# Kernel tuning notes

Measured on AMD Instinct MI355X. Metric: run time of the kernel, lower is better.

Reference implementation:

```python
import jax, jax.numpy as jnp
import numpy as np

N_NODES = 100000
N_EDGES = 1600000
IN_DIM, H1, H2, OUT_DIM = 128, 64, 32, 16


def setup_inputs() -> dict:
    key = jax.random.key(0)
    ks = jax.random.split(key, 9)
    x = jax.random.normal(ks[0], (N_NODES, IN_DIM), dtype=jnp.float32)
    edge_index = jax.random.randint(ks[1], (2, N_EDGES), 0, N_NODES, dtype=jnp.int64)
    # nn.Linear-style params (out_feats, in_feats) + bias
    def lin(k, o, i):
        bound = 1.0 / np.sqrt(i)
        kw, kb = jax.random.split(k)
        W = jax.random.uniform(kw, (o, i), jnp.float32, -bound, bound)
        b = jax.random.uniform(kb, (o,), jnp.float32, -bound, bound)
        return W, b
    W1, b1 = lin(ks[2], H1, IN_DIM)
    W2, b2 = lin(ks[3], H2, H1)
    Wf, bf = lin(ks[4], OUT_DIM, H2)
    return {"x": x, "edge_index": edge_index, "W1": W1, "b1": b1,
            "W2": W2, "b2": b2, "Wf": Wf, "bf": bf}


def reference(x, edge_index, W1, b1, W2, b2, Wf, bf):
    # Original: adj = to_dense_adj(edge_index); graph built from adj.T; DGL
    # copy_src+sum then gives new_h[src] = sum over dst of h[dst], i.e. A @ h
    # with A[src, dst]. No activation between layers (unused in forward),
    # dropout inactive at inference.
    N = x.shape[0]
    src, dst = edge_index[0], edge_index[1]

    def aggregate(h):  # sum of out-neighbor features: [N, d]
        return jax.ops.segment_sum(h[dst], src, num_segments=N)

    h = aggregate(x) @ W1.T + b1          # [N, 64]
    h = aggregate(h) @ W2.T + b2          # [N, 32]
    pooled = jnp.max(h, axis=0)           # [32] global max pool over nodes
    return pooled @ Wf.T + bf             # [16]
```

## Files before the change

### kernel.cpp

```cpp
#include <hip/hip_runtime.h>

#define N_NODES 100000
#define N_EDGES 1600000
#define IN_DIM 128
#define H1_DIM 64
#define H2_DIM 32
#define OUT_DIM 16

#define NPB 64
#define KB 1563
#define OFFW (KB + 1)
#define NCH 256
#define CH_E (N_EDGES / NCH)
#define CAP2 1536
#define NBIN1 64
#define NBIN2 (NCH - NBIN1)
#define NGB 782

typedef __attribute__((ext_vector_type(8))) short short8;
typedef __attribute__((ext_vector_type(4))) float f32x4;

__device__ inline unsigned short f2b(float v) {
    unsigned u = __float_as_uint(v);
    u += 0x7FFF + ((u >> 16) & 1);
    return (unsigned short)(u >> 16);
}
__device__ inline short f2bs(float v) { return (short)f2b(v); }
__device__ inline unsigned f32_to_key(float v) {
    unsigned u = __float_as_uint(v);
    return (v >= 0.f) ? (u | 0x80000000u) : ~u;
}
__device__ __forceinline__ void acc8(float* a, uint4 v) {
    a[0] += __uint_as_float(v.x << 16);
    a[1] += __uint_as_float(v.x & 0xFFFF0000u);
    a[2] += __uint_as_float(v.y << 16);
    a[3] += __uint_as_float(v.y & 0xFFFF0000u);
    a[4] += __uint_as_float(v.z << 16);
    a[5] += __uint_as_float(v.z & 0xFFFF0000u);
    a[6] += __uint_as_float(v.w << 16);
    a[7] += __uint_as_float(v.w & 0xFFFF0000u);
}

__device__ __forceinline__ void bin_chunk(const int* __restrict__ src,
                                          const int* __restrict__ dst,
                                          unsigned* __restrict__ off,
                                          unsigned* __restrict__ grec, int c) {
    __shared__ int hist[2048];
    __shared__ int part[512];
    __shared__ int cur[2048];
    int t = threadIdx.x;
    int e0 = c * CH_E;
    for (int i = t; i < 2048; i += 512) hist[i] = 0;
    __syncthreads();
    for (int e = t; e < CH_E; e += 512) atomicAdd(&hist[src[e0 + e] >> 6], 1);
    __syncthreads();
    int h0 = hist[4 * t], h1 = hist[4 * t + 1], h2 = hist[4 * t + 2], h3 = hist[4 * t + 3];
    int tot = h0 + h1 + h2 + h3;
    part[t] = tot;
    __syncthreads();
    for (int o = 1; o < 512; o <<= 1) {
        int a = (t >= o) ? part[t - o] : 0;
        __syncthreads();
        part[t] += a;
        __syncthreads();
    }
    int gb = part[t] - tot;
    int o0 = gb, o1 = gb + h0, o2 = o1 + h1, o3 = o2 + h2;
    int b4 = 4 * t;
    cur[b4] = o0; cur[b4 + 1] = o1; cur[b4 + 2] = o2; cur[b4 + 3] = o3;
    if (b4 + 0 < KB) off[(size_t)c * OFFW + b4 + 0] = o0;
    if (b4 + 1 < KB) off[(size_t)c * OFFW + b4 + 1] = o1;
    if (b4 + 2 < KB) off[(size_t)c * OFFW + b4 + 2] = o2;
    if (b4 + 3 < KB) off[(size_t)c * OFFW + b4 + 3] = o3;
    if (t == 0) off[(size_t)c * OFFW + KB] = CH_E;
    __syncthreads();
    for (int e = t; e < CH_E; e += 512) {
        int s = src[e0 + e];
        int d = dst[e0 + e];
        int p = atomicAdd(&cur[s >> 6], 1);
        grec[(size_t)e0 + p] = ((unsigned)(s & 63) << 17) | (unsigned)d;
    }
}

__global__ __launch_bounds__(512) void k1_kernel(const int* __restrict__ src,
                                                 const int* __restrict__ dst,
                                                 unsigned* __restrict__ off,
                                                 unsigned* __restrict__ grec,
                                                 const float* __restrict__ W1,
                                                 const float* __restrict__ W2,
                                                 unsigned short* __restrict__ Wcb) {
    if (blockIdx.x < NBIN1) {
        bin_chunk(src, dst, off, grec, blockIdx.x);
        return;
    }
    int t = threadIdx.x;
    for (int idx = t; idx < H2_DIM * IN_DIM; idx += 512) {
        int j = idx >> 7, f = idx & 127;
        float acc = 0.f;
        for (int k = 0; k < H1_DIM; ++k)
            acc += W2[j * H1_DIM + k] * W1[k * IN_DIM + f];
        Wcb[idx] = f2b(acc);
    }
}

__global__ __launch_bounds__(512) void k2_kernel(const int* __restrict__ src,
                                                 const int* __restrict__ dst,
                                                 unsigned* __restrict__ off,
                                                 unsigned* __restrict__ grec,
                                                 const float* __restrict__ x,
                                                 const unsigned short* __restrict__ Wcb,
                                                 unsigned short* __restrict__ yb) {
    if (blockIdx.x < NBIN2) {
        bin_chunk(src, dst, off, grec, NBIN1 + blockIdx.x);
        return;
    }
    int gb = blockIdx.x - NBIN2;
    int t = threadIdx.x;
    int w = t >> 6, l = t & 63;
    int row = l & 15, kg = l >> 4;
    int base = gb * 128 + w * 16;
    int node = base + row;
    int nclamp = (node < N_NODES) ? node : (N_NODES - 1);
    const float* xp = x + (size_t)nclamp * IN_DIM + kg * 8;
    const unsigned short* b0p = Wcb + (size_t)row * IN_DIM + kg * 8;
    const unsigned short* b1p = Wcb + (size_t)(16 + row) * IN_DIM + kg * 8;
    f32x4 acc0 = {0.f, 0.f, 0.f, 0.f}, acc1 = {0.f, 0.f, 0.f, 0.f};
#pragma unroll
    for (int kk = 0; kk < 4; ++kk) {
        float4 xa = *(const float4*)(xp + kk * 32);
        float4 xb = *(const float4*)(xp + kk * 32 + 4);
        short8 a;
        a[0] = f2bs(xa.x); a[1] = f2bs(xa.y); a[2] = f2bs(xa.z); a[3] = f2bs(xa.w);
        a[4] = f2bs(xb.x); a[5] = f2bs(xb.y); a[6] = f2bs(xb.z); a[7] = f2bs(xb.w);
        short8 b0 = *(const short8*)(b0p + kk * 32);
        short8 b1 = *(const short8*)(b1p + kk * 32);
        acc0 = __builtin_amdgcn_mfma_f32_16x16x32_bf16(a, b0, acc0, 0, 0, 0);
        acc1 = __builtin_amdgcn_mfma_f32_16x16x32_bf16(a, b1, acc1, 0, 0, 0);
    }
#pragma unroll
    for (int r = 0; r < 4; ++r) {
        int n2 = base + kg * 4 + r;
        if (n2 < N_NODES) {
            yb[(size_t)n2 * H2_DIM + row]      = f2b(acc0[r]);
            yb[(size_t)n2 * H2_DIM + 16 + row] = f2b(acc1[r]);
        }
    }
}

template <int ROUND>
__global__ __launch_bounds__(256) void agg_kernel(const unsigned short* __restrict__ in,
                                                  const unsigned* __restrict__ off,
                                                  const unsigned* __restrict__ grec,
                                                  unsigned* __restrict__ grec2,
                                                  unsigned* __restrict__ noff,
                                                  unsigned short* __restrict__ z1b,
                                                  const float* __restrict__ W2,
                                                  const float* __restrict__ b1,
                                                  const float* __restrict__ b2,
                                                  unsigned* __restrict__ pk) {
    __shared__ int len[NCH], pos[NCH], sst[NCH];
    __shared__ int shist[64], scur2[64];
    __shared__ int sscan[65];
    __shared__ unsigned rbuf[CAP2];
    __shared__ unsigned sbuf[CAP2];
    __shared__ float smq[16][4][8];
    __shared__ float scv[32], sb2v[32];
    __shared__ int s_cnt;
    int t = threadIdx.x;
    int b = blockIdx.x;
    int gid = t >> 4;
    int L = t & 15;
    int chunk = L & 3, subset = L >> 2;

    if (ROUND == 1) {
        {
            unsigned o0 = off[(size_t)t * OFFW + b];
            unsigned o1 = off[(size_t)t * OFFW + b + 1];
            sst[t] = (int)o0;
            len[t] = (int)(o1 - o0);
            pos[t] = (int)(o1 - o0);
        }
        __syncthreads();
        for (int o = 1; o < NCH; o <<= 1) {
            int a = (t >= o) ? pos[t - o] : 0;
            __syncthreads();
            pos[t] += a;
            __syncthreads();
        }
        pos[t] -= len[t];
        if (t == NCH - 1) s_cnt = min(pos[t] + len[t], CAP2);
        __syncthreads();
        for (int c = gid; c < NCH; c += 16) {
            int Ln = len[c], P = pos[c], S = sst[c];
            for (int k = L; k < Ln; k += 16) {
                int q = P + k;
                if (q < CAP2) rbuf[q] = grec[(size_t)c * CH_E + S + k];
            }
        }
        if (t < 64) shist[t] = 0;
        __syncthreads();
        int cnt = s_cnt;
        for (int i = t; i < cnt; i += 256) atomicAdd(&shist[rbuf[i] >> 17], 1);
        __syncthreads();
        if (t < 64) scur2[t] = shist[t];
        __syncthreads();
        for (int o = 1; o < 64; o <<= 1) {
            int a = (t < 64 && t >= o) ? scur2[t - o] : 0;
            __syncthreads();
            if (t < 64) scur2[t] += a;
            __syncthreads();
        }
        if (t < 64) sscan[t] = scur2[t] - shist[t];
        if (t == 63) sscan[64] = scur2[63];
        __syncthreads();
        if (t < 64) scur2[t] = sscan[t];
        __syncthreads();
        for (int i = t; i < cnt; i += 256) {
            unsigned r = rbuf[i];
            int p = atomicAdd(&scur2[r >> 17], 1);
            if (p < CAP2) sbuf[p] = r;
        }
        __syncthreads();
        for (int i = t; i < cnt; i += 256) grec2[(size_t)b * CAP2 + i] = sbuf[i];
        if (t < 65) noff[(size_t)b * 65 + t] = (unsigned)sscan[t];
    } else {
        if (t < 65) sscan[t] = (int)noff[(size_t)b * 65 + t];
        __syncthreads();
        int cnt = sscan[64];
        for (int i = t; i < cnt; i += 256) sbuf[i] = grec2[(size_t)b * CAP2 + i];
        if (t < 32) {
            float s = 0.f;
            for (int k = 0; k < H1_DIM; ++k) s += W2[t * H1_DIM + k] * b1[k];
            scv[t] = s;
            sb2v[t] = b2[t];
        }
    }
    __syncthreads();

    float cfv[8], bbv[8], m[8];
    if (ROUND == 2) {
#pragma unroll
        for (int j = 0; j < 8; ++j) {
            cfv[j] = scv[chunk * 8 + j];
            bbv[j] = sb2v[chunk * 8 + j];
            m[j] = -3.402823466e+38f;
        }
    }

    for (int sl = gid; sl < NPB; sl += 16) {
        int r0 = sscan[sl], r1 = sscan[sl + 1];
        float a[8] = {0.f, 0.f, 0.f, 0.f, 0.f, 0.f, 0.f, 0.f};
        float aa[8] = {0.f, 0.f, 0.f, 0.f, 0.f, 0.f, 0.f, 0.f};
        for (int e = r0; e < r1; e += 8) {
            int eA = e + subset, eB = e + 4 + subset;
            if (eA < r1) {
                unsigned rc = sbuf[eA];
                uint4 v = *(const uint4*)(in + (size_t)(rc & 0x1FFFFu) * H2_DIM + chunk * 8);
                acc8(a, v);
            }
            if (eB < r1) {
                unsigned rc = sbuf[eB];
                uint4 v = *(const uint4*)(in + (size_t)(rc & 0x1FFFFu) * H2_DIM + chunk * 8);
                acc8(aa, v);
            }
        }
#pragma unroll
        for (int j = 0; j < 8; ++j) {
            float s = a[j] + aa[j];
            s += __shfl_xor(s, 4);
            s += __shfl_xor(s, 8);
            a[j] = s;
        }
        int node = b * NPB + sl;
        if (node < N_NODES) {
            if (ROUND == 1) {
                if (subset == 0) {
                    uint4 o;
                    o.x = (unsigned)f2b(a[0]) | ((unsigned)f2b(a[1]) << 16);
                    o.y = (unsigned)f2b(a[2]) | ((unsigned)f2b(a[3]) << 16);
                    o.z = (unsigned)f2b(a[4]) | ((unsigned)f2b(a[5]) << 16);
                    o.w = (unsigned)f2b(a[6]) | ((unsigned)f2b(a[7]) << 16);
                    *(uint4*)(z1b + (size_t)node * H2_DIM + chunk * 8) = o;
                }
            } else {
                float dg = (float)(r1 - r0);
#pragma unroll
                for (int j = 0; j < 8; ++j)
                    m[j] = fmaxf(m[j], a[j] + dg * cfv[j] + bbv[j]);
            }
        }
    }
    if (ROUND == 2) {
        if (subset == 0) {
#pragma unroll
            for (int j = 0; j < 8; ++j) smq[gid][chunk][j] = m[j];
        }
        __syncthreads();
        if (t < 32) {
            int c = t >> 3, j = t & 7;
            float mm = smq[0][c][j];
#pragma unroll
            for (int k = 1; k < 16; ++k) mm = fmaxf(mm, smq[k][c][j]);
            atomicMax(&pk[t], f32_to_key(mm));
        }
    }
}

__global__ void final_kernel(const unsigned* __restrict__ pk,
                             const float* __restrict__ Wf,
                             const float* __restrict__ bfv,
                             float* __restrict__ out) {
    __shared__ float pooled[H2_DIM];
    int t = threadIdx.x;
    if (t < H2_DIM) {
        unsigned k = pk[t];
        unsigned u = (k & 0x80000000u) ? (k & 0x7FFFFFFFu) : ~k;
        pooled[t] = __uint_as_float(u);
    }
    __syncthreads();
    if (t < OUT_DIM) {
        float acc = bfv[t];
        for (int j = 0; j < H2_DIM; ++j)
            acc += Wf[t * H2_DIM + j] * pooled[j];
        out[t] = acc;
    }
}

extern "C" void kernel_launch(void* const* d_in, const int* in_sizes, int n_in,
                              void* d_out, int out_size, void* d_ws, size_t ws_size,
                              hipStream_t stream) {
    const float* x  = (const float*)d_in[0];
    const int*   ei = (const int*)d_in[1];
    const float* W1 = (const float*)d_in[2];
    const float* b1 = (const float*)d_in[3];
    const float* W2 = (const float*)d_in[4];
    const float* b2 = (const float*)d_in[5];
    const float* Wf = (const float*)d_in[6];
    const float* bf = (const float*)d_in[7];
    float* out = (float*)d_out;

    const int* src = ei;
    const int* dst = ei + N_EDGES;

    unsigned short* yb  = (unsigned short*)d_ws;
    unsigned short* z1b = yb + (size_t)N_NODES * H2_DIM;
    unsigned short* Wcb = z1b + (size_t)N_NODES * H2_DIM;
    unsigned* pk    = (unsigned*)(Wcb + H2_DIM * IN_DIM);
    unsigned* off   = pk + H2_DIM;
    unsigned* grec  = off + (size_t)NCH * OFFW;
    unsigned* grec2 = grec + N_EDGES;
    unsigned* noff  = grec2 + (size_t)KB * CAP2;

    hipMemsetAsync(pk, 0, H2_DIM * sizeof(unsigned), stream);

    k1_kernel<<<NBIN1 + 1, 512, 0, stream>>>(src, dst, off, grec, W1, W2, Wcb);
    k2_kernel<<<NBIN2 + NGB, 512, 0, stream>>>(src, dst, off, grec, x, Wcb, yb);

    agg_kernel<1><<<KB, 256, 0, stream>>>(yb, off, grec, grec2, noff, z1b,
                                          nullptr, nullptr, nullptr, pk);
    agg_kernel<2><<<KB, 256, 0, stream>>>(z1b, off, grec, grec2, noff, nullptr,
                                          W2, b1, b2, pk);

    final_kernel<<<1, 64, 0, stream>>>(pk, Wf, bf, out);
}
```

Before: 118.6 us.

## Fuse final projection into last aggregation block and widen gather unroll

```diff
diff --git a/kernel.cpp b/kernel.cpp
--- a/kernel.cpp
+++ b/kernel.cpp
@@ -157,7 +157,11 @@
                                                   const float* __restrict__ W2,
                                                   const float* __restrict__ b1,
                                                   const float* __restrict__ b2,
-                                                  unsigned* __restrict__ pk) {
+                                                  const float* __restrict__ Wf,
+                                                  const float* __restrict__ bfv,
+                                                  unsigned* __restrict__ pk,
+                                                  unsigned* __restrict__ done,
+                                                  float* __restrict__ out) {
     __shared__ int len[NCH], pos[NCH], sst[NCH];
     __shared__ int shist[64], scur2[64];
     __shared__ int sscan[65];
@@ -166,6 +170,7 @@
     __shared__ float smq[16][4][8];
     __shared__ float scv[32], sb2v[32];
     __shared__ int s_cnt;
+    __shared__ unsigned s_ticket;
     int t = threadIdx.x;
     int b = blockIdx.x;
     int gid = t >> 4;
@@ -249,44 +254,57 @@
 
     for (int sl = gid; sl < NPB; sl += 16) {
         int r0 = sscan[sl], r1 = sscan[sl + 1];
-        float a[8] = {0.f, 0.f, 0.f, 0.f, 0.f, 0.f, 0.f, 0.f};
-        float aa[8] = {0.f, 0.f, 0.f, 0.f, 0.f, 0.f, 0.f, 0.f};
-        for (int e = r0; e < r1; e += 8) {
-            int eA = e + subset, eB = e + 4 + subset;
-            if (eA < r1) {
-                unsigned rc = sbuf[eA];
+        float a0[8] = {0.f, 0.f, 0.f, 0.f, 0.f, 0.f, 0.f, 0.f};
+        float a1[8] = {0.f, 0.f, 0.f, 0.f, 0.f, 0.f, 0.f, 0.f};
+        float a2[8] = {0.f, 0.f, 0.f, 0.f, 0.f, 0.f, 0.f, 0.f};
+        float a3[8] = {0.f, 0.f, 0.f, 0.f, 0.f, 0.f, 0.f, 0.f};
+        for (int e = r0; e < r1; e += 16) {
+            int e0 = e + subset, e1 = e + 4 + subset;
+            int e2 = e + 8 + subset, e3 = e + 12 + subset;
+            if (e0 < r1) {
+                unsigned rc = sbuf[e0];
                 uint4 v = *(const uint4*)(in + (size_t)(rc & 0x1FFFFu) * H2_DIM + chunk * 8);
-                acc8(a, v);
-            }
-            if (eB < r1) {
-                unsigned rc = sbuf[eB];
+                acc8(a0, v);
+            }
+            if (e1 < r1) {
+                unsigned rc = sbuf[e1];
                 uint4 v = *(const uint4*)(in + (size_t)(rc & 0x1FFFFu) * H2_DIM + chunk * 8);
-                acc8(aa, v);
+                acc8(a1, v);
+            }
+            if (e2 < r1) {
+                unsigned rc = sbuf[e2];
+                uint4 v = *(const uint4*)(in + (size_t)(rc & 0x1FFFFu) * H2_DIM + chunk * 8);
+                acc8(a2, v);
+            }
+            if (e3 < r1) {
+                unsigned rc = sbuf[e3];
+                uint4 v = *(const uint4*)(in + (size_t)(rc & 0x1FFFFu) * H2_DIM + chunk * 8);
+                acc8(a3, v);
             }
         }
 #pragma unroll
         for (int j = 0; j < 8; ++j) {
-            float s = a[j] + aa[j];
+            float s = (a0[j] + a1[j]) + (a2[j] + a3[j]);
             s += __shfl_xor(s, 4);
             s += __shfl_xor(s, 8);
-            a[j] = s;
+            a0[j] = s;
         }
         int node = b * NPB + sl;
         if (node < N_NODES) {
             if (ROUND == 1) {
                 if (subset == 0) {
                     uint4 o;
-                    o.x = (unsigned)f2b(a[0]) | ((unsigned)f2b(a[1]) << 16);
-                    o.y = (unsigned)f2b(a[2]) | ((unsigned)f2b(a[3]) << 16);
-                    o.z = (unsigned)f2b(a[4]) | ((unsigned)f2b(a[5]) << 16);
-                    o.w = (unsigned)f2b(a[6]) | ((unsigned)f2b(a[7]) << 16);
+                    o.x = (unsigned)f2b(a0[0]) | ((unsigned)f2b(a0[1]) << 16);
+                    o.y = (unsigned)f2b(a0[2]) | ((unsigned)f2b(a0[3]) << 16);
+                    o.z = (unsigned)f2b(a0[4]) | ((unsigned)f2b(a0[5]) << 16);
+                    o.w = (unsigned)f2b(a0[6]) | ((unsigned)f2b(a0[7]) << 16);
                     *(uint4*)(z1b + (size_t)node * H2_DIM + chunk * 8) = o;
                 }
             } else {
                 float dg = (float)(r1 - r0);
 #pragma unroll
                 for (int j = 0; j < 8; ++j)
-                    m[j] = fmaxf(m[j], a[j] + dg * cfv[j] + bbv[j]);
+                    m[j] = fmaxf(m[j], a0[j] + dg * cfv[j] + bbv[j]);
             }
         }
     }
@@ -303,26 +321,24 @@
             for (int k = 1; k < 16; ++k) mm = fmaxf(mm, smq[k][c][j]);
             atomicMax(&pk[t], f32_to_key(mm));
         }
-    }
-}
-
-__global__ void final_kernel(const unsigned* __restrict__ pk,
-                             const float* __restrict__ Wf,
-                             const float* __restrict__ bfv,
-                             float* __restrict__ out) {
-    __shared__ float pooled[H2_DIM];
-    int t = threadIdx.x;
-    if (t < H2_DIM) {
-        unsigned k = pk[t];
-        unsigned u = (k & 0x80000000u) ? (k & 0x7FFFFFFFu) : ~k;
-        pooled[t] = __uint_as_float(u);
-    }
-    __syncthreads();
-    if (t < OUT_DIM) {
-        float acc = bfv[t];
-        for (int j = 0; j < H2_DIM; ++j)
-            acc += Wf[t * H2_DIM + j] * pooled[j];
-        out[t] = acc;
+        __threadfence();
+        __syncthreads();
+        if (t == 0) s_ticket = atomicAdd(done, 1u);
+        __syncthreads();
+        if (s_ticket == KB - 1) {
+            if (t < 32) {
+                unsigned k = atomicMax(&pk[t], 0u);
+                unsigned u = (k & 0x80000000u) ? (k & 0x7FFFFFFFu) : ~k;
+                scv[t] = __uint_as_float(u);
+            }
+            __syncthreads();
+            if (t < OUT_DIM) {
+                float acc = bfv[t];
+                for (int j = 0; j < H2_DIM; ++j)
+                    acc += Wf[t * H2_DIM + j] * scv[j];
+                out[t] = acc;
+            }
+        }
     }
 }
 
@@ -346,20 +362,20 @@
     unsigned short* z1b = yb + (size_t)N_NODES * H2_DIM;
     unsigned short* Wcb = z1b + (size_t)N_NODES * H2_DIM;
     unsigned* pk    = (unsigned*)(Wcb + H2_DIM * IN_DIM);
-    unsigned* off   = pk + H2_DIM;
+    unsigned* done  = pk + H2_DIM;
+    unsigned* off   = done + 1;
     unsigned* grec  = off + (size_t)NCH * OFFW;
     unsigned* grec2 = grec + N_EDGES;
     unsigned* noff  = grec2 + (size_t)KB * CAP2;
 
-    hipMemsetAsync(pk, 0, H2_DIM * sizeof(unsigned), stream);
+    hipMemsetAsync(pk, 0, (H2_DIM + 1) * sizeof(unsigned), stream);
 
     k1_kernel<<<NBIN1 + 1, 512, 0, stream>>>(src, dst, off, grec, W1, W2, Wcb);
     k2_kernel<<<NBIN2 + NGB, 512, 0, stream>>>(src, dst, off, grec, x, Wcb, yb);
 
     agg_kernel<1><<<KB, 256, 0, stream>>>(yb, off, grec, grec2, noff, z1b,
-                                          nullptr, nullptr, nullptr, pk);
+                                          nullptr, nullptr, nullptr,
+                                          nullptr, nullptr, pk, done, nullptr);
     agg_kernel<2><<<KB, 256, 0, stream>>>(z1b, off, grec, grec2, noff, nullptr,
-                                          W2, b1, b2, pk);
-
-    final_kernel<<<1, 64, 0, stream>>>(pk, Wf, bf, out);
-}
+                                          W2, b1, b2, Wf, bf, pk, done, out);
+}
```

Measured after the change: 218.7 us. +84.4%, slower.

## Merge binning and projection kernels, fuse final linear via last-block ticket

Applied to the files above, without the earlier changes.

```diff
diff --git a/kernel.cpp b/kernel.cpp
--- a/kernel.cpp
+++ b/kernel.cpp
@@ -13,8 +13,6 @@
 #define NCH 256
 #define CH_E (N_EDGES / NCH)
 #define CAP2 1536
-#define NBIN1 64
-#define NBIN2 (NCH - NBIN1)
 #define NGB 782
 
 typedef __attribute__((ext_vector_type(8))) short short8;
@@ -82,48 +80,37 @@
     }
 }
 
-__global__ __launch_bounds__(512) void k1_kernel(const int* __restrict__ src,
+__global__ __launch_bounds__(512) void ka_kernel(const int* __restrict__ src,
                                                  const int* __restrict__ dst,
                                                  unsigned* __restrict__ off,
                                                  unsigned* __restrict__ grec,
+                                                 const float* __restrict__ x,
                                                  const float* __restrict__ W1,
                                                  const float* __restrict__ W2,
-                                                 unsigned short* __restrict__ Wcb) {
-    if (blockIdx.x < NBIN1) {
+                                                 unsigned short* __restrict__ yb) {
+    __shared__ unsigned short wl[H2_DIM * 136];
+    if (blockIdx.x < NCH) {
         bin_chunk(src, dst, off, grec, blockIdx.x);
         return;
     }
+    int gb = blockIdx.x - NCH;
     int t = threadIdx.x;
     for (int idx = t; idx < H2_DIM * IN_DIM; idx += 512) {
         int j = idx >> 7, f = idx & 127;
         float acc = 0.f;
         for (int k = 0; k < H1_DIM; ++k)
             acc += W2[j * H1_DIM + k] * W1[k * IN_DIM + f];
-        Wcb[idx] = f2b(acc);
-    }
-}
-
-__global__ __launch_bounds__(512) void k2_kernel(const int* __restrict__ src,
-                                                 const int* __restrict__ dst,
-                                                 unsigned* __restrict__ off,
-                                                 unsigned* __restrict__ grec,
-                                                 const float* __restrict__ x,
-                                                 const unsigned short* __restrict__ Wcb,
-                                                 unsigned short* __restrict__ yb) {
-    if (blockIdx.x < NBIN2) {
-        bin_chunk(src, dst, off, grec, NBIN1 + blockIdx.x);
-        return;
-    }
-    int gb = blockIdx.x - NBIN2;
-    int t = threadIdx.x;
+        wl[j * 136 + f] = f2b(acc);
+    }
+    __syncthreads();
     int w = t >> 6, l = t & 63;
     int row = l & 15, kg = l >> 4;
     int base = gb * 128 + w * 16;
     int node = base + row;
     int nclamp = (node < N_NODES) ? node : (N_NODES - 1);
     const float* xp = x + (size_t)nclamp * IN_DIM + kg * 8;
-    const unsigned short* b0p = Wcb + (size_t)row * IN_DIM + kg * 8;
-    const unsigned short* b1p = Wcb + (size_t)(16 + row) * IN_DIM + kg * 8;
+    const unsigned short* b0p = wl + row * 136 + kg * 8;
+    const unsigned short* b1p = wl + (16 + row) * 136 + kg * 8;
     f32x4 acc0 = {0.f, 0.f, 0.f, 0.f}, acc1 = {0.f, 0.f, 0.f, 0.f};
 #pragma unroll
     for (int kk = 0; kk < 4; ++kk) {
@@ -157,7 +144,11 @@
                                                   const float* __restrict__ W2,
                                                   const float* __restrict__ b1,
                                                   const float* __restrict__ b2,
-                                                  unsigned* __restrict__ pk) {
+                                                  const float* __restrict__ Wf,
+                                                  const float* __restrict__ bfv,
+                                                  unsigned* __restrict__ pk,
+                                                  unsigned* __restrict__ done,
+                                                  float* __restrict__ out) {
     __shared__ int len[NCH], pos[NCH], sst[NCH];
     __shared__ int shist[64], scur2[64];
     __shared__ int sscan[65];
@@ -166,6 +157,7 @@
     __shared__ float smq[16][4][8];
     __shared__ float scv[32], sb2v[32];
     __shared__ int s_cnt;
+    __shared__ unsigned s_ticket;
     int t = threadIdx.x;
     int b = blockIdx.x;
     int gid = t >> 4;
@@ -303,26 +295,24 @@
             for (int k = 1; k < 16; ++k) mm = fmaxf(mm, smq[k][c][j]);
             atomicMax(&pk[t], f32_to_key(mm));
         }
-    }
-}
-
-__global__ void final_kernel(const unsigned* __restrict__ pk,
-                             const float* __restrict__ Wf,
-                             const float* __restrict__ bfv,
-                             float* __restrict__ out) {
-    __shared__ float pooled[H2_DIM];
-    int t = threadIdx.x;
-    if (t < H2_DIM) {
-        unsigned k = pk[t];
-        unsigned u = (k & 0x80000000u) ? (k & 0x7FFFFFFFu) : ~k;
-        pooled[t] = __uint_as_float(u);
-    }
-    __syncthreads();
-    if (t < OUT_DIM) {
-        float acc = bfv[t];
-        for (int j = 0; j < H2_DIM; ++j)
-            acc += Wf[t * H2_DIM + j] * pooled[j];
-        out[t] = acc;
+        __threadfence();
+        __syncthreads();
+        if (t == 0) s_ticket = atomicAdd(done, 1u);
+        __syncthreads();
+        if (s_ticket == KB - 1) {
+            if (t < 32) {
+                unsigned k = atomicMax(&pk[t], 0u);
+                unsigned u = (k & 0x80000000u) ? (k & 0x7FFFFFFFu) : ~k;
+                scv[t] = __uint_as_float(u);
+            }
+            __syncthreads();
+            if (t < OUT_DIM) {
+                float acc = bfv[t];
+                for (int j = 0; j < H2_DIM; ++j)
+                    acc += Wf[t * H2_DIM + j] * scv[j];
+                out[t] = acc;
+            }
+        }
     }
 }
 
@@ -344,22 +334,20 @@
 
     unsigned short* yb  = (unsigned short*)d_ws;
     unsigned short* z1b = yb + (size_t)N_NODES * H2_DIM;
-    unsigned short* Wcb = z1b + (size_t)N_NODES * H2_DIM;
-    unsigned* pk    = (unsigned*)(Wcb + H2_DIM * IN_DIM);
-    unsigned* off   = pk + H2_DIM;
+    unsigned* pk    = (unsigned*)(z1b + (size_t)N_NODES * H2_DIM);
+    unsigned* done  = pk + H2_DIM;
+    unsigned* off   = done + 1;
     unsigned* grec  = off + (size_t)NCH * OFFW;
     unsigned* grec2 = grec + N_EDGES;
     unsigned* noff  = grec2 + (size_t)KB * CAP2;
 
-    hipMemsetAsync(pk, 0, H2_DIM * sizeof(unsigned), stream);
-
-    k1_kernel<<<NBIN1 + 1, 512, 0, stream>>>(src, dst, off, grec, W1, W2, Wcb);
-    k2_kernel<<<NBIN2 + NGB, 512, 0, stream>>>(src, dst, off, grec, x, Wcb, yb);
+    hipMemsetAsync(pk, 0, (H2_DIM + 1) * sizeof(unsigned), stream);
+
+    ka_kernel<<<NCH + NGB, 512, 0, stream>>>(src, dst, off, grec, x, W1, W2, yb);
 
     agg_kernel<1><<<KB, 256, 0, stream>>>(yb, off, grec, grec2, noff, z1b,
-                                          nullptr, nullptr, nullptr, pk);
+                                          nullptr, nullptr, nullptr,
+                                          nullptr, nullptr, pk, done, nullptr);
     agg_kernel<2><<<KB, 256, 0, stream>>>(z1b, off, grec, grec2, noff, nullptr,
-                                          W2, b1, b2, pk);
-
-    final_kernel<<<1, 64, 0, stream>>>(pk, Wf, bf, out);
-}
+                                          W2, b1, b2, Wf, bf, pk, done, out);
+}
```

Result: slower. 244.6 us (+106.2%).
